# Optimization experiments

Hardware: AMD Instinct MI355X
Metric: run time of the kernel (lower is better)

## Reference

```python
import jax, jax.numpy as jnp
import numpy as np

B = 8
N_PER = 8192   # xyz points per batch
M_PER = 2048   # query points per batch
C_FEAT = 32
RADIUS = 0.2
K = 32         # sample_nums
USE_XYZ = True


def setup_inputs() -> dict:
    key = jax.random.key(0)
    k1, k2, k3 = jax.random.split(key, 3)
    xyz = jax.random.uniform(k1, (B * N_PER, 3), dtype=jnp.float32)
    new_xyz = jax.random.uniform(k2, (B * M_PER, 3), dtype=jnp.float32)
    features = jax.random.normal(k3, (B * N_PER, C_FEAT), dtype=jnp.float32)
    xyz_batch_cnt = jnp.full((B,), N_PER, dtype=jnp.int32)
    new_xyz_batch_cnt = jnp.full((B,), M_PER, dtype=jnp.int32)
    return {
        "xyz": xyz,
        "xyz_batch_cnt": xyz_batch_cnt,
        "new_xyz": new_xyz,
        "new_xyz_batch_cnt": new_xyz_batch_cnt,
        "features": features,
    }


def _ball_query(xyz_b, new_b, radius, k):
    # xyz_b: (B, N, 3), new_b: (B, M, 3)
    n = xyz_b.shape[1]
    # squared pairwise distances (B, M, N)
    d2 = jnp.sum((new_b[:, :, None, :] - xyz_b[:, None, :, :]) ** 2, axis=-1)
    mask = d2 < (radius * radius)
    # first-k in-radius indices (CUDA ball_query keeps neighbors in point order)
    scores = jnp.where(mask, jnp.arange(n, dtype=jnp.int32), jnp.int32(n))
    idx_sorted = jnp.sort(scores, axis=-1)[..., :k]          # (B, M, k)
    cnt = jnp.sum(mask, axis=-1)                              # (B, M)
    empty = cnt == 0                                          # (B, M)
    first = idx_sorted[..., :1]                               # duplicate first hit
    slot = jnp.arange(k, dtype=jnp.int32)
    idx = jnp.where(slot[None, None, :] < cnt[..., None], idx_sorted, first)
    idx = jnp.where(empty[..., None], jnp.int32(0), idx)      # empty balls -> 0
    return idx, empty


def reference(xyz, xyz_batch_cnt, new_xyz, new_xyz_batch_cnt, features):
    b = xyz_batch_cnt.shape[0]
    xyz_b = xyz.reshape(b, -1, 3)          # (B, N, 3)
    new_b = new_xyz.reshape(b, -1, 3)      # (B, M, 3)
    feat_b = features.reshape(b, xyz_b.shape[1], -1)  # (B, N, C)

    idx, empty = _ball_query(xyz_b, new_b, RADIUS, K)  # (B, M, K), (B, M)

    gather = jax.vmap(lambda pts, i: pts[i])           # per-batch gather
    grouped_xyz = gather(xyz_b, idx) - new_b[:, :, None, :]   # (B, M, K, 3)
    grouped_xyz = jnp.where(empty[..., None, None], 0.0, grouped_xyz)

    grouped_feat = gather(feat_b, idx)                        # (B, M, K, C)
    grouped_feat = jnp.where(empty[..., None, None], 0.0, grouped_feat)

    if USE_XYZ:
        new_features = jnp.concatenate([grouped_xyz, grouped_feat], axis=-1)
    else:
        new_features = grouped_feat
    # (B, M, K, 3+C) -> (B*M, 3+C, K) to match torch (Mtot, C', nsample)
    m_tot = b * new_b.shape[1]
    new_features = jnp.transpose(new_features, (0, 1, 3, 2)).reshape(
        m_tot, -1, K)
    idx_flat = idx.reshape(m_tot, K)
    return new_features, idx_flat
```

## Files before the change

kernel.cpp:

```cpp
#include <hip/hip_runtime.h>

#define BATCHES   8
#define N_PER     8192
#define M_PER     2048
#define C_FEAT    32
#define KNN       32
#define R2        0.04f
#define M_TOT     (BATCHES * M_PER)
#define FEAT_OUT  (3 + C_FEAT)
#define OUT_FEAT_SZ ((size_t)M_TOT * FEAT_OUT * KNN)

__global__ __launch_bounds__(256) void ballquery_kernel(
    const float* __restrict__ xyz,
    const float* __restrict__ new_xyz,
    float* __restrict__ out)
{
    __shared__ int sidx[4][KNN];

    const int wave = threadIdx.x >> 6;
    const int lane = threadIdx.x & 63;
    const int q    = blockIdx.x * 4 + wave;
    const int b    = q >> 11;
    const int base = b * N_PER;

    const float px = new_xyz[q * 3 + 0];
    const float py = new_xyz[q * 3 + 1];
    const float pz = new_xyz[q * 3 + 2];

    const unsigned long long below = (1ull << lane) - 1ull;

    int cnt = 0;
    int first = 0;

    const float* p0 = xyz + (size_t)(base + lane) * 3;
    float x0 = p0[0], y0 = p0[1], z0 = p0[2];
    float x1 = p0[192], y1 = p0[193], z1 = p0[194];

    for (int cb = 0;;) {
        const int nb = cb + 128;
        const bool more = nb < N_PER;
        float ax0 = 0.f, ay0 = 0.f, az0 = 0.f, ax1 = 0.f, ay1 = 0.f, az1 = 0.f;
        if (more) {
            const float* pn = xyz + (size_t)(base + nb + lane) * 3;
            ax0 = pn[0];   ay0 = pn[1];   az0 = pn[2];
            ax1 = pn[192]; ay1 = pn[193]; az1 = pn[194];
        }

        const float dx0 = px - x0, dy0 = py - y0, dz0 = pz - z0;
        const float dx1 = px - x1, dy1 = py - y1, dz1 = pz - z1;
        const float d20 = __fadd_rn(__fadd_rn(__fmul_rn(dx0, dx0),
                                              __fmul_rn(dy0, dy0)),
                                    __fmul_rn(dz0, dz0));
        const float d21 = __fadd_rn(__fadd_rn(__fmul_rn(dx1, dx1),
                                              __fmul_rn(dy1, dy1)),
                                    __fmul_rn(dz1, dz1));
        const bool in0 = d20 < R2;
        const bool in1 = d21 < R2;
        const unsigned long long m0 = __ballot(in0);
        const unsigned long long m1 = __ballot(in1);

        if (cnt == 0) {
            if (m0)      first = cb + (__ffsll((long long)m0) - 1);
            else if (m1) first = cb + 64 + (__ffsll((long long)m1) - 1);
        }
        const int c0 = __popcll(m0);
        if (in0) {
            const int r = cnt + __popcll(m0 & below);
            if (r < KNN) sidx[wave][r] = cb + lane;
        }
        if (in1) {
            const int r = cnt + c0 + __popcll(m1 & below);
            if (r < KNN) sidx[wave][r] = cb + 64 + lane;
        }
        cnt += c0 + __popcll(m1);

        if (cnt >= KNN || !more) break;
        x0 = ax0; y0 = ay0; z0 = az0;
        x1 = ax1; y1 = ay1; z1 = az1;
        cb = nb;
    }

    const int pad = (cnt == 0) ? 0 : first;
    if (lane < KNN) {
        const int li = (lane < cnt) ? sidx[wave][lane] : pad;
        float f = (float)li;
        if (cnt == 0) f = -0.0f;
        out[OUT_FEAT_SZ + (size_t)q * KNN + lane] = f;
    }
}

__global__ __launch_bounds__(256) void group_kernel(
    const float* __restrict__ xyz,
    const float* __restrict__ new_xyz,
    const float* __restrict__ features,
    float* __restrict__ out)
{
    const int tid = blockIdx.x * 256 + threadIdx.x;
    const int q   = tid >> 5;
    const int k   = tid & 31;
    const int b   = q >> 11;
    const int base = b * N_PER;

    const float fidx = out[OUT_FEAT_SZ + (size_t)q * KNN + k];
    const bool empty = (__float_as_uint(fidx) >> 31) != 0;
    const float zf   = empty ? 0.0f : 1.0f;
    const int li     = (int)fidx;
    const int gi     = base + li;

    const float px = new_xyz[q * 3 + 0];
    const float py = new_xyz[q * 3 + 1];
    const float pz = new_xyz[q * 3 + 2];

    const float gx = xyz[(size_t)gi * 3 + 0] - px;
    const float gy = xyz[(size_t)gi * 3 + 1] - py;
    const float gz = xyz[(size_t)gi * 3 + 2] - pz;

    float* o = out + (size_t)q * (FEAT_OUT * KNN);
    o[0 * KNN + k] = zf * gx;
    o[1 * KNN + k] = zf * gy;
    o[2 * KNN + k] = zf * gz;

    const float4* f = (const float4*)(features + (size_t)gi * C_FEAT);
    #pragma unroll
    for (int j4 = 0; j4 < C_FEAT / 4; ++j4) {
        const float4 v = f[j4];
        o[(3 + j4 * 4 + 0) * KNN + k] = zf * v.x;
        o[(3 + j4 * 4 + 1) * KNN + k] = zf * v.y;
        o[(3 + j4 * 4 + 2) * KNN + k] = zf * v.z;
        o[(3 + j4 * 4 + 3) * KNN + k] = zf * v.w;
    }
}

extern "C" void kernel_launch(void* const* d_in, const int* in_sizes, int n_in,
                              void* d_out, int out_size, void* d_ws, size_t ws_size,
                              hipStream_t stream) {
    const float* xyz      = (const float*)d_in[0];
    const float* new_xyz  = (const float*)d_in[2];
    const float* features = (const float*)d_in[4];
    float* out = (float*)d_out;

    ballquery_kernel<<<M_TOT / 4, 256, 0, stream>>>(xyz, new_xyz, out);
    group_kernel<<<(M_TOT * KNN) / 256, 256, 0, stream>>>(xyz, new_xyz, features, out);
}
```

Before: 135.7 us.

## Fuse ball query and grouping into one kernel with shared-memory indices

Merges the ball-query and grouping kernels into a single launch. Each wave keeps its neighbor indices in shared memory and gathers the features directly, with the two half-waves each handling 16 channels. This removes the second launch and the round trip of indices through global memory, and uses readfirstlane and mbcnt intrinsics to trim scalar and rank-computation work. The trade-off is that gather work now rides on the ball-query waves with only 4 queries per block, which may reduce gather parallelism. The empty-ball index output changes from -0.0 to 0.0, which is numerically the same value.

```diff
diff --git a/kernel.cpp b/kernel.cpp
--- a/kernel.cpp
+++ b/kernel.cpp
@@ -10,16 +10,17 @@
 #define FEAT_OUT  (3 + C_FEAT)
 #define OUT_FEAT_SZ ((size_t)M_TOT * FEAT_OUT * KNN)
 
-__global__ __launch_bounds__(256) void ballquery_kernel(
+__global__ __launch_bounds__(256) void sqag_fused_kernel(
     const float* __restrict__ xyz,
     const float* __restrict__ new_xyz,
+    const float* __restrict__ features,
     float* __restrict__ out)
 {
     __shared__ int sidx[4][KNN];
 
     const int wave = threadIdx.x >> 6;
     const int lane = threadIdx.x & 63;
-    const int q    = blockIdx.x * 4 + wave;
+    const int q    = __builtin_amdgcn_readfirstlane(blockIdx.x * 4 + wave);
     const int b    = q >> 11;
     const int base = b * N_PER;
 
@@ -27,21 +28,18 @@
     const float py = new_xyz[q * 3 + 1];
     const float pz = new_xyz[q * 3 + 2];
 
-    const unsigned long long below = (1ull << lane) - 1ull;
-
     int cnt = 0;
     int first = 0;
 
-    const float* p0 = xyz + (size_t)(base + lane) * 3;
-    float x0 = p0[0], y0 = p0[1], z0 = p0[2];
-    float x1 = p0[192], y1 = p0[193], z1 = p0[194];
+    const float* p = xyz + (size_t)base * 3 + lane * 3;
+    float x0 = p[0],   y0 = p[1],   z0 = p[2];
+    float x1 = p[192], y1 = p[193], z1 = p[194];
 
     for (int cb = 0;;) {
-        const int nb = cb + 128;
-        const bool more = nb < N_PER;
+        const bool more = (cb + 128) < N_PER;
+        const float* pn = p + 384;
         float ax0 = 0.f, ay0 = 0.f, az0 = 0.f, ax1 = 0.f, ay1 = 0.f, az1 = 0.f;
         if (more) {
-            const float* pn = xyz + (size_t)(base + nb + lane) * 3;
             ax0 = pn[0];   ay0 = pn[1];   az0 = pn[2];
             ax1 = pn[192]; ay1 = pn[193]; az1 = pn[194];
         }
@@ -54,81 +52,84 @@
         const float d21 = __fadd_rn(__fadd_rn(__fmul_rn(dx1, dx1),
                                               __fmul_rn(dy1, dy1)),
                                     __fmul_rn(dz1, dz1));
-        const bool in0 = d20 < R2;
-        const bool in1 = d21 < R2;
-        const unsigned long long m0 = __ballot(in0);
-        const unsigned long long m1 = __ballot(in1);
+        const unsigned long long m0 = __ballot(d20 < R2);
+        const unsigned long long m1 = __ballot(d21 < R2);
 
         if (cnt == 0) {
             if (m0)      first = cb + (__ffsll((long long)m0) - 1);
             else if (m1) first = cb + 64 + (__ffsll((long long)m1) - 1);
         }
         const int c0 = __popcll(m0);
-        if (in0) {
-            const int r = cnt + __popcll(m0 & below);
-            if (r < KNN) sidx[wave][r] = cb + lane;
-        }
-        if (in1) {
-            const int r = cnt + c0 + __popcll(m1 & below);
-            if (r < KNN) sidx[wave][r] = cb + 64 + lane;
+        {
+            const unsigned r0 = __builtin_amdgcn_mbcnt_hi(
+                (unsigned)(m0 >> 32),
+                __builtin_amdgcn_mbcnt_lo((unsigned)m0, 0u));
+            const unsigned r1 = __builtin_amdgcn_mbcnt_hi(
+                (unsigned)(m1 >> 32),
+                __builtin_amdgcn_mbcnt_lo((unsigned)m1, 0u));
+            if (d20 < R2) {
+                const int r = cnt + (int)r0;
+                if (r < KNN) sidx[wave][r] = cb + lane;
+            }
+            if (d21 < R2) {
+                const int r = cnt + c0 + (int)r1;
+                if (r < KNN) sidx[wave][r] = cb + 64 + lane;
+            }
         }
         cnt += c0 + __popcll(m1);
 
         if (cnt >= KNN || !more) break;
+        p = pn;
+        cb += 128;
         x0 = ax0; y0 = ay0; z0 = az0;
         x1 = ax1; y1 = ay1; z1 = az1;
-        cb = nb;
     }
 
     const int pad = (cnt == 0) ? 0 : first;
-    if (lane < KNN) {
-        const int li = (lane < cnt) ? sidx[wave][lane] : pad;
-        float f = (float)li;
-        if (cnt == 0) f = -0.0f;
-        out[OUT_FEAT_SZ + (size_t)q * KNN + lane] = f;
-    }
-}
+    if (lane >= cnt && lane < KNN) sidx[wave][lane] = pad;
+    const float zf = (cnt == 0) ? 0.0f : 1.0f;
 
-__global__ __launch_bounds__(256) void group_kernel(
-    const float* __restrict__ xyz,
-    const float* __restrict__ new_xyz,
-    const float* __restrict__ features,
-    float* __restrict__ out)
-{
-    const int tid = blockIdx.x * 256 + threadIdx.x;
-    const int q   = tid >> 5;
-    const int k   = tid & 31;
-    const int b   = q >> 11;
-    const int base = b * N_PER;
+    const int k    = lane & 31;
+    const int half = lane >> 5;
 
-    const float fidx = out[OUT_FEAT_SZ + (size_t)q * KNN + k];
-    const bool empty = (__float_as_uint(fidx) >> 31) != 0;
-    const float zf   = empty ? 0.0f : 1.0f;
-    const int li     = (int)fidx;
-    const int gi     = base + li;
+    const int li = sidx[wave][k];
+    const int gi = base + li;
 
-    const float px = new_xyz[q * 3 + 0];
-    const float py = new_xyz[q * 3 + 1];
-    const float pz = new_xyz[q * 3 + 2];
+    const float4* f = (const float4*)(features + (size_t)gi * C_FEAT + half * 16);
+    const float4 v0 = f[0];
+    const float4 v1 = f[1];
+    const float4 v2 = f[2];
+    const float4 v3 = f[3];
 
     const float gx = xyz[(size_t)gi * 3 + 0] - px;
     const float gy = xyz[(size_t)gi * 3 + 1] - py;
     const float gz = xyz[(size_t)gi * 3 + 2] - pz;
 
     float* o = out + (size_t)q * (FEAT_OUT * KNN);
-    o[0 * KNN + k] = zf * gx;
-    o[1 * KNN + k] = zf * gy;
-    o[2 * KNN + k] = zf * gz;
+    if (half == 0) {
+        o[0 * KNN + k] = zf * gx;
+        o[1 * KNN + k] = zf * gy;
+        o[2 * KNN + k] = zf * gz;
+        out[OUT_FEAT_SZ + (size_t)q * KNN + k] = (float)li;
+    }
 
-    const float4* f = (const float4*)(features + (size_t)gi * C_FEAT);
-    #pragma unroll
-    for (int j4 = 0; j4 < C_FEAT / 4; ++j4) {
-        const float4 v = f[j4];
-        o[(3 + j4 * 4 + 0) * KNN + k] = zf * v.x;
-        o[(3 + j4 * 4 + 1) * KNN + k] = zf * v.y;
-        o[(3 + j4 * 4 + 2) * KNN + k] = zf * v.z;
-        o[(3 + j4 * 4 + 3) * KNN + k] = zf * v.w;
-    }
+    const int jb = 3 + half * 16;
+    o[(jb +  0) * KNN + k] = zf * v0.x;
+    o[(jb +  1) * KNN + k] = zf * v0.y;
+    o[(jb +  2) * KNN + k] = zf * v0.z;
+    o[(jb +  3) * KNN + k] = zf * v0.w;
+    o[(jb +  4) * KNN + k] = zf * v1.x;
+    o[(jb +  5) * KNN + k] = zf * v1.y;
+    o[(jb +  6) * KNN + k] = zf * v1.z;
+    o[(jb +  7) * KNN + k] = zf * v1.w;
+    o[(jb +  8) * KNN + k] = zf * v2.x;
+    o[(jb +  9) * KNN + k] = zf * v2.y;
+    o[(jb + 10) * KNN + k] = zf * v2.z;
+    o[(jb + 11) * KNN + k] = zf * v2.w;
+    o[(jb + 12) * KNN + k] = zf * v3.x;
+    o[(jb + 13) * KNN + k] = zf * v3.y;
+    o[(jb + 14) * KNN + k] = zf * v3.z;
+    o[(jb + 15) * KNN + k] = zf * v3.w;
 }
 
 extern "C" void kernel_launch(void* const* d_in, const int* in_sizes, int n_in,
@@ -139,6 +140,5 @@
     const float* features = (const float*)d_in[4];
     float* out = (float*)d_out;
 
-    ballquery_kernel<<<M_TOT / 4, 256, 0, stream>>>(xyz, new_xyz, out);
-    group_kernel<<<(M_TOT * KNN) / 256, 256, 0, stream>>>(xyz, new_xyz, features, out);
+    sqag_fused_kernel<<<M_TOT / 4, 256, 0, stream>>>(xyz, new_xyz, features, out);
 }
```

After: 134.4 us. No clear change (-1.0%).
